# Performance work log

Measured on AMD Instinct MI355X. Metric: run time of the kernel, lower is better.

## Reference

```python
import jax, jax.numpy as jnp
from jax import lax
import numpy as np

D_IN = 512    # inputdim
HID = 128     # hiddendim
D_INNER = 2 * HID   # 256
D_PROJ = 2 * D_INNER  # 512
N_STATE = 16
R_DT = 8      # ceil(128/16)
B, H, W = 8, 32, 32


def _layernorm(y, g, b):
    mu = y.mean(-1, keepdims=True)
    var = ((y - mu) ** 2).mean(-1, keepdims=True)
    return (y - mu) / jnp.sqrt(var + 1e-5) * g + b


def _ssm(x, xw, dtw, dtb, Al, Dv, g, be):
    # x: [B, D, L] -> y: [B, L, D]  (Mamba selective scan, delta_softplus=True)
    Bb, D, L = x.shape
    n = Al.shape[1]
    xd = jnp.einsum('bdl,kd->blk', x, xw)             # [B,L,R+2N]
    dts = xd[..., :R_DT]
    Bs = xd[..., R_DT:R_DT + n]                        # [B,L,N]
    Cs = xd[..., R_DT + n:]                            # [B,L,N]
    delta = jax.nn.softplus(jnp.einsum('blr,dr->bld', dts, dtw) + dtb)  # [B,L,D]
    A = -jnp.exp(Al)                                   # [D,N]
    xt = x.transpose(0, 2, 1)                          # [B,L,D]
    dA = jnp.exp(delta[..., None] * A)                 # [B,L,D,N]
    dBx = delta[..., None] * Bs[:, :, None, :] * xt[..., None]  # [B,L,D,N]

    def step(h, inp):
        da, dbx, c = inp
        h = h * da + dbx
        return h, jnp.einsum('bdn,bn->bd', h, c)

    h0 = jnp.zeros((Bb, D, n), x.dtype)
    _, ys = lax.scan(step, h0, (dA.transpose(1, 0, 2, 3),
                                dBx.transpose(1, 0, 2, 3),
                                Cs.transpose(1, 0, 2)))
    y = ys.transpose(1, 0, 2) + xt * Dv                # [B,L,D]
    return _layernorm(y, g, be)


def _up2(y, h, w):
    Bb, L, C = y.shape
    img = y.transpose(0, 2, 1).reshape(Bb, C, h, w)
    img = jnp.repeat(jnp.repeat(img, 2, axis=2), 2, axis=3)
    return img.reshape(Bb, C, 4 * L).transpose(0, 2, 1)


def _conv1x1(x, w, b):
    return jnp.einsum('bchw,oc->bohw', x, w) + b[None, :, None, None]


def _conv2s2(x, w, b):
    out = lax.conv_general_dilated(x, w, (2, 2), 'VALID',
                                   dimension_numbers=('NCHW', 'OIHW', 'NCHW'))
    return out + b[None, :, None, None]


def _forward(input_f, in_w, in_b, c1_w, c1_b, c2_w, c2_b, c3_w, c3_b, out_w, out_b,
             xw1, dtw1, dtb1, Al1, Dv1, g1, be1,
             xw2, dtw2, dtb2, Al2, Dv2, g2, be2,
             xw3, dtw3, dtb3, Al3, Dv3, g3, be3):
    xz = _conv1x1(input_f, in_w, in_b)
    x, z = jnp.split(xz, 2, axis=1)
    f1 = _conv1x1(x, c1_w, c1_b)                      # [B,256,H,W]
    f2 = _conv2s2(f1, c2_w, c2_b)                     # [B,256,H/2,W/2]
    f3 = _conv2s2(f2, c3_w, c3_b)                     # [B,256,H/4,W/4]

    Bb, C, h3, w3 = f3.shape
    fx3 = f3.reshape(Bb, C, h3 * w3)
    y3 = _ssm(fx3, xw3, dtw3, dtb3, Al3, Dv3, g3, be3) + \
         jnp.flip(_ssm(jnp.flip(fx3, -1), xw3, dtw3, dtb3, Al3, Dv3, g3, be3), 1)
    y2_ = _up2(y3, h3, w3)

    _, _, h2, w2 = f2.shape
    fx2 = f2.reshape(Bb, C, h2 * w2)
    y2 = _ssm(fx2, xw2, dtw2, dtb2, Al2, Dv2, g2, be2) + \
         jnp.flip(_ssm(jnp.flip(fx2, -1), xw2, dtw2, dtb2, Al2, Dv2, g2, be2), 1) + y2_
    y1_ = _up2(y2, h2, w2)

    _, _, h1, w1 = f1.shape
    fx1 = f1.reshape(Bb, C, h1 * w1)
    # NOTE: source uses fssm1 forward and fssm2 on the flipped sequence
    y1 = _ssm(fx1, xw1, dtw1, dtb1, Al1, Dv1, g1, be1) + \
         jnp.flip(_ssm(jnp.flip(fx1, -1), xw2, dtw2, dtb2, Al2, Dv2, g2, be2), 1) + y1_

    out1 = y1.transpose(0, 2, 1).reshape(Bb, C, h1, w1)
    out = out1 * jax.nn.silu(z)
    return _conv1x1(out, out_w, out_b)


def setup_inputs() -> dict:
    key = jax.random.key(0)
    ks = iter(jax.random.split(key, 64))
    def nrm(shape, s=0.05):
        return (jax.random.normal(next(ks), shape, dtype=jnp.float32) * s)
    inp = {
        'input_f': jax.random.normal(next(ks), (B, D_IN, H, W), dtype=jnp.float32),
        'in_w': nrm((D_PROJ, D_IN)), 'in_b': nrm((D_PROJ,)),
        'c1_w': nrm((D_INNER, D_INNER)), 'c1_b': nrm((D_INNER,)),
        'c2_w': nrm((D_INNER, D_INNER, 2, 2)), 'c2_b': nrm((D_INNER,)),
        'c3_w': nrm((D_INNER, D_INNER, 2, 2)), 'c3_b': nrm((D_INNER,)),
        'out_w': nrm((D_IN, D_INNER)), 'out_b': nrm((D_IN,)),
    }
    Al = jnp.log(jnp.tile(jnp.arange(1, N_STATE + 1, dtype=jnp.float32), (D_INNER, 1)))
    for i in (1, 2, 3):
        inp[f'xw{i}'] = nrm((R_DT + 2 * N_STATE, D_INNER))
        inp[f'dtw{i}'] = nrm((D_INNER, R_DT), s=R_DT ** -0.5)
        inp[f'dtb{i}'] = nrm((D_INNER,)) - 4.0   # inv-softplus of small dt
        inp[f'Al{i}'] = Al
        inp[f'Dv{i}'] = jnp.ones((D_INNER,), jnp.float32)
        inp[f'g{i}'] = jnp.ones((D_INNER,), jnp.float32)
        inp[f'be{i}'] = jnp.zeros((D_INNER,), jnp.float32)
    return inp


def reference(input_f, in_w, in_b, c1_w, c1_b, c2_w, c2_b, c3_w, c3_b, out_w, out_b,
              xw1, dtw1, dtb1, Al1, Dv1, g1, be1,
              xw2, dtw2, dtb2, Al2, Dv2, g2, be2,
              xw3, dtw3, dtb3, Al3, Dv3, g3, be3):
    return _forward(input_f, in_w, in_b, c1_w, c1_b, c2_w, c2_b, c3_w, c3_b, out_w, out_b,
                    xw1, dtw1, dtb1, Al1, Dv1, g1, be1,
                    xw2, dtw2, dtb2, Al2, Dv2, g2, be2,
                    xw3, dtw3, dtb3, Al3, Dv3, g3, be3)
```

## Files before the change

kernel.cpp:

```cpp
#include <hip/hip_runtime.h>
#include <cstddef>

#define DEV static __device__ __forceinline__

typedef __attribute__((ext_vector_type(8))) short short8;
typedef __attribute__((ext_vector_type(4))) float floatx4;

DEV float siluf(float v) { return v / (1.f + expf(-v)); }

DEV unsigned short f2bf(float f) {
  unsigned int u = __float_as_uint(f);
  u += 0x7fff + ((u >> 16) & 1);
  return (unsigned short)(u >> 16);
}
DEV float bf2f(unsigned short u) {
  return __uint_as_float(((unsigned int)u) << 16);
}
DEV float4 bf2f4(ushort4 v) {
  return make_float4(bf2f(v.x), bf2f(v.y), bf2f(v.z), bf2f(v.w));
}

template <int CTRL>
DEV float qadd(float v) {
  int s = __builtin_amdgcn_update_dpp(__float_as_int(v), __float_as_int(v),
                                      CTRL, 0xF, 0xF, false);
  return v + __int_as_float(s);
}

__global__ __launch_bounds__(256) void prep_k(
    const float* __restrict__ in_w, const float* __restrict__ c1_w,
    const float* __restrict__ c2_w, const float* __restrict__ c3_w,
    const float* __restrict__ out_w, const float* __restrict__ xw1,
    const float* __restrict__ xw2, const float* __restrict__ xw3,
    unsigned short* __restrict__ wsW,
    const float* __restrict__ input_f, unsigned short* __restrict__ inT,
    const float* __restrict__ in_b, const float* __restrict__ c1_b,
    unsigned short* __restrict__ w_fz, float* __restrict__ bias_fz)
{
  __shared__ float tile[32][33];
  __shared__ float c1s[1024];
  __shared__ float part[32][8];
  int bid = blockIdx.x;
  int t = threadIdx.x;
  if (bid < 3960) {
    int gid = bid * 256 + t;
    float v;
    if      (gid < 262144)  v = in_w[gid];
    else if (gid < 327680)  v = c1_w[gid - 262144];
    else if (gid < 589824)  {
      int off = gid - 327680;
      int o = off >> 10, kk = off & 1023, ij = kk >> 8, c = kk & 255;
      v = c2_w[o * 1024 + c * 4 + ij];
    }
    else if (gid < 851968)  {
      int off = gid - 589824;
      int o = off >> 10, kk = off & 1023, ij = kk >> 8, c = kk & 255;
      v = c3_w[o * 1024 + c * 4 + ij];
    }
    else if (gid < 983040)  v = out_w[gid - 851968];
    else if (gid < 993280)  v = xw1[gid - 983040];
    else if (gid < 1003520) v = xw2[gid - 993280];
    else                    v = xw3[gid - 1003520];
    wsW[gid] = f2bf(v);
  } else if (bid < 8056) {
    int idx = bid - 3960;
    int b = idx >> 9, blk = idx & 511;
    int pt = blk & 31, ct = blk >> 5;
    int p0 = pt * 32, c0 = ct * 32;
    int r = t >> 5, cc = t & 31;
#pragma unroll
    for (int i = 0; i < 4; i++) {
      int row = r + 8 * i;
      tile[row][cc] = input_f[((size_t)b * 512 + c0 + row) * 1024 + p0 + cc];
    }
    __syncthreads();
#pragma unroll
    for (int i = 0; i < 4; i++) {
      int row = r + 8 * i;
      inT[((size_t)b * 1024 + p0 + row) * 512 + c0 + cc] = f2bf(tile[cc][row]);
    }
  } else if (bid < 8184) {
    int ib = bid - 8056;
    int ot = ib >> 1;
    int ci = ((ib & 1) << 8) + t;
#pragma unroll
    for (int rr = 0; rr < 4; rr++)
      c1s[rr * 256 + t] = c1_w[(size_t)(ot * 4 + rr) * 256 + t];
    __syncthreads();
    float acc[4] = {0.f, 0.f, 0.f, 0.f};
#pragma unroll 4
    for (int m = 0; m < 256; m++) {
      float wv = in_w[(size_t)m * 512 + ci];
#pragma unroll
      for (int rr = 0; rr < 4; rr++) acc[rr] += c1s[rr * 256 + m] * wv;
    }
#pragma unroll
    for (int rr = 0; rr < 4; rr++)
      w_fz[(size_t)(ot * 4 + rr) * 512 + ci] = f2bf(acc[rr]);
  } else if (bid < 8192) {
    int jb = bid - 8184;
    int oo = t >> 3, mc = t & 7;
    int o = jb * 32 + oo;
    float s = 0.f;
#pragma unroll 8
    for (int mm = 0; mm < 32; mm++) {
      int m = mc * 32 + mm;
      s += c1_w[(size_t)o * 256 + m] * in_b[m];
    }
    part[oo][mc] = s;
    __syncthreads();
    if (mc == 0) {
      float a = c1_b[o];
#pragma unroll
      for (int k = 0; k < 8; k++) a += part[oo][k];
      bias_fz[o] = a;
    }
    if (jb == 0) bias_fz[256 + t] = in_b[256 + t];
  } else {
    int r = bid - 8192;
    const float* src = in_w + (size_t)(256 + r) * 512;
    w_fz[(size_t)(256 + r) * 512 + t]       = f2bf(src[t]);
    w_fz[(size_t)(256 + r) * 512 + 256 + t] = f2bf(src[256 + t]);
  }
}

template <int EPI>
DEV void mgemm_body(const unsigned short* __restrict__ A, long long sA,
                    const unsigned short* __restrict__ B, long long sB,
                    const float* __restrict__ bias,
                    void* __restrict__ O1, void* __restrict__ O2,
                    void* __restrict__ O3,
                    int M, int N, int K, int Mt, int Nt, int bid)
{
  __shared__ __align__(16) unsigned short Ab[2 * 128 * 40];
  __shared__ __align__(16) unsigned short Bb[2 * 128 * 40];
  int tiles = Mt * Nt;
  int bb = bid / tiles;
  int rr = bid - bb * tiles;
  int m0 = (rr / Nt) * 128;
  int n0 = (rr % Nt) * 128;
  const unsigned short* Ap = A + (size_t)bb * sA;
  const unsigned short* Bp = B + (size_t)bb * sB;

  int t = threadIdx.x;
  int lane = t & 63;
  int wm = ((t >> 7) & 1) * 64;
  int wn = ((t >> 6) & 1) * 64;
  int l15 = lane & 15, quad = lane >> 4;

  int srow = t >> 1;
  int shalf = (t & 1) * 16;
  int arow = m0 + srow; if (arow > M - 1) arow = M - 1;
  int brow = n0 + srow; if (brow > N - 1) brow = N - 1;
  const unsigned short* ap = Ap + (size_t)arow * K + shalf;
  const unsigned short* bp = Bp + (size_t)brow * K + shalf;
  unsigned short* as = &Ab[srow * 40 + shalf];
  unsigned short* bs = &Bb[srow * 40 + shalf];

  floatx4 acc[4][4] = {};

  uint4 a0 = *(const uint4*)(ap);
  uint4 a1 = *(const uint4*)(ap + 8);
  uint4 b0 = *(const uint4*)(bp);
  uint4 b1 = *(const uint4*)(bp + 8);
  *(uint4*)as = a0; *(uint4*)(as + 8) = a1;
  *(uint4*)bs = b0; *(uint4*)(bs + 8) = b1;
  __syncthreads();
  int cur = 0;
  for (int k0 = 0; k0 < K; k0 += 32) {
    bool last = (k0 + 32 >= K);
    if (!last) {
      a0 = *(const uint4*)(ap + k0 + 32);
      a1 = *(const uint4*)(ap + k0 + 40);
      b0 = *(const uint4*)(bp + k0 + 32);
      b1 = *(const uint4*)(bp + k0 + 40);
    }
    int co = cur * 5120;
    short8 af[4], bfr[4];
#pragma unroll
    for (int i = 0; i < 4; i++)
      af[i] = *(const short8*)&Ab[co + (wm + i * 16 + l15) * 40 + quad * 8];
#pragma unroll
    for (int j = 0; j < 4; j++)
      bfr[j] = *(const short8*)&Bb[co + (wn + j * 16 + l15) * 40 + quad * 8];
#pragma unroll
    for (int i = 0; i < 4; i++)
#pragma unroll
      for (int j = 0; j < 4; j++)
        acc[i][j] = __builtin_amdgcn_mfma_f32_16x16x32_bf16(af[i], bfr[j],
                                                            acc[i][j], 0, 0, 0);
    if (!last) {
      int no = 5120 - co;
      *(uint4*)(as + no) = a0; *(uint4*)(as + no + 8) = a1;
      *(uint4*)(bs + no) = b0; *(uint4*)(bs + no + 8) = b1;
      __syncthreads();
      cur ^= 1;
    }
  }

  if (EPI == 1) {
    unsigned short* F1t = (unsigned short*)O1;
    unsigned short* F1b = (unsigned short*)O2;
    unsigned short* Sz  = (unsigned short*)O3;
    float bn[4]; int nn[4];
#pragma unroll
    for (int j = 0; j < 4; j++) { nn[j] = n0 + wn + j * 16 + l15; bn[j] = bias[nn[j]]; }
#pragma unroll
    for (int i = 0; i < 4; i++) {
      int pixb = m0 + wm + i * 16 + quad * 4;
#pragma unroll
      for (int j = 0; j < 4; j++) {
        int n = nn[j];
        float vr[4];
#pragma unroll
        for (int r = 0; r < 4; r++) vr[r] = acc[i][j][r] + bn[j];
        if (n < 256) {
#pragma unroll
          for (int r = 0; r < 4; r++)
            F1t[((size_t)bb * 1024 + pixb + r) * 256 + n] = f2bf(vr[r]);
          ushort4 o4;
          o4.x = f2bf(vr[0]); o4.y = f2bf(vr[1]); o4.z = f2bf(vr[2]); o4.w = f2bf(vr[3]);
          *(ushort4*)&F1b[((size_t)bb * 256 + n) * 1024 + pixb] = o4;
        } else {
#pragma unroll
          for (int r = 0; r < 4; r++)
            Sz[((size_t)bb * 1024 + pixb + r) * 256 + (n - 256)] =
                f2bf(siluf(vr[r]));
        }
      }
    }
  } else {
#pragma unroll
    for (int i = 0; i < 4; i++) {
      int m = m0 + wm + i * 16 + quad * 4;
#pragma unroll
      for (int j = 0; j < 4; j++) {
        int n = n0 + wn + j * 16 + l15;
        if (m < M && n < N) {
          float vr[4];
#pragma unroll
          for (int r = 0; r < 4; r++)
            vr[r] = acc[i][j][r] + (bias ? bias[m + r] : 0.f);
          float* Y0 = (float*)O1;
          float* yp = &Y0[((size_t)bb * M + m) * N + n];
#pragma unroll
          for (int r = 0; r < 4; r++) yp[(size_t)r * N] = vr[r];
        }
      }
    }
  }
}

template <int EPI>
__global__ __launch_bounds__(256) void mgemm_k(
    const unsigned short* __restrict__ A, long long sA,
    const unsigned short* __restrict__ B, long long sB,
    const float* __restrict__ bias, void* __restrict__ O1, void* __restrict__ O2,
    void* __restrict__ O3,
    int M, int N, int K, int Mt, int Nt)
{
  mgemm_body<EPI>(A, sA, B, sB, bias, O1, O2, O3, M, N, K, Mt, Nt, blockIdx.x);
}

__global__ __launch_bounds__(256) void cgemm_k(
    const unsigned short* __restrict__ A,
    const unsigned short* __restrict__ B, long long sB,
    const float* __restrict__ bias,
    unsigned short* __restrict__ O1, unsigned short* __restrict__ O2,
    int M, int N, int K, int Mt, int Nt)
{
  __shared__ __align__(16) unsigned short Ab[2][64 * 72];
  __shared__ __align__(16) unsigned short Bb[2][32 * 72];
  int bid = blockIdx.x;
  int tiles = Mt * Nt;
  int bb = bid / tiles;
  int rr = bid - bb * tiles;
  int m0 = (rr / Nt) * 64;
  int n0 = (rr % Nt) * 32;
  const unsigned short* Bp = B + (size_t)bb * sB;

  int t = threadIdx.x, lane = t & 63;
  int wm = ((t >> 7) & 1) * 32;
  int wn = ((t >> 6) & 1) * 16;
  int l15 = lane & 15, quad = lane >> 4;

  int ar = t >> 2, ac = (t & 3) * 16;
  int brc = (t >> 2) & 31, bc = (t & 3) * 16;
  const unsigned short* apc = A + (size_t)(m0 + ar) * K + ac;
  const unsigned short* bpc = Bp + (size_t)(n0 + brc) * K + bc;

  floatx4 acc2[2] = {};

  uint4 av0 = *(const uint4*)(apc);
  uint4 av1 = *(const uint4*)(apc + 8);
  uint4 bv0 = {}, bv1 = {};
  if (t < 128) { bv0 = *(const uint4*)(bpc); bv1 = *(const uint4*)(bpc + 8); }
  {
    unsigned short* asc = &Ab[0][0] + ar * 72 + ac;
    *(uint4*)asc = av0; *(uint4*)(asc + 8) = av1;
    if (t < 128) {
      unsigned short* bsc = &Bb[0][0] + brc * 72 + bc;
      *(uint4*)bsc = bv0; *(uint4*)(bsc + 8) = bv1;
    }
  }
  __syncthreads();
  int cur = 0;
  for (int k0 = 0; k0 < K; k0 += 64) {
    bool last = (k0 + 64 >= K);
    if (!last) {
      av0 = *(const uint4*)(apc + k0 + 64);
      av1 = *(const uint4*)(apc + k0 + 72);
      if (t < 128) {
        bv0 = *(const uint4*)(bpc + k0 + 64);
        bv1 = *(const uint4*)(bpc + k0 + 72);
      }
    }
    const unsigned short* Ac = &Ab[cur][0];
    const unsigned short* Bc = &Bb[cur][0];
    short8 afc[2][2], bfc[2];
#pragma unroll
    for (int i = 0; i < 2; i++)
#pragma unroll
      for (int kk = 0; kk < 2; kk++)
        afc[i][kk] = *(const short8*)&Ac[(wm + i * 16 + l15) * 72 + kk * 32 + quad * 8];
#pragma unroll
    for (int kk = 0; kk < 2; kk++)
      bfc[kk] = *(const short8*)&Bc[(wn + l15) * 72 + kk * 32 + quad * 8];
#pragma unroll
    for (int kk = 0; kk < 2; kk++) {
      acc2[0] = __builtin_amdgcn_mfma_f32_16x16x32_bf16(afc[0][kk], bfc[kk], acc2[0], 0, 0, 0);
      acc2[1] = __builtin_amdgcn_mfma_f32_16x16x32_bf16(afc[1][kk], bfc[kk], acc2[1], 0, 0, 0);
    }
    if (!last) {
      unsigned short* asn = &Ab[cur ^ 1][0] + ar * 72 + ac;
      *(uint4*)asn = av0; *(uint4*)(asn + 8) = av1;
      if (t < 128) {
        unsigned short* bsn = &Bb[cur ^ 1][0] + brc * 72 + bc;
        *(uint4*)bsn = bv0; *(uint4*)(bsn + 8) = bv1;
      }
      __syncthreads();
      cur ^= 1;
    }
  }

#pragma unroll
  for (int i = 0; i < 2; i++) {
    int m = m0 + wm + i * 16 + quad * 4;
    int n = n0 + wn + l15;
    float vr[4];
#pragma unroll
    for (int r = 0; r < 4; r++) vr[r] = acc2[i][r] + bias[m + r];
#pragma unroll
    for (int r = 0; r < 4; r++)
      O1[((size_t)bb * M + m + r) * N + n] = f2bf(vr[r]);
    ushort4 o;
    o.x = f2bf(vr[0]); o.y = f2bf(vr[1]); o.z = f2bf(vr[2]); o.w = f2bf(vr[3]);
    *(ushort4*)&O2[((size_t)bb * N + n) * M + m] = o;
  }
}

__global__ __launch_bounds__(256) void fat1_k(
    const unsigned short* __restrict__ w_xw12, const unsigned short* __restrict__ f1t,
    float* __restrict__ xd12, unsigned short* __restrict__ ic2)
{
  int bid = blockIdx.x;
  if (bid < 64) {
    mgemm_body<0>(w_xw12, 0, f1t, 1024 * 256, nullptr, xd12, nullptr, nullptr,
                  80, 1024, 256, 1, 8, bid);
  } else {
    int idx = (bid - 64) * 256 + threadIdx.x;
    int cs = idx & 31, ij = (idx >> 5) & 3, n = (idx >> 7) & 255, b = idx >> 15;
    int i = ij >> 1, j = ij & 1;
    int y = n >> 4, x = n & 15;
    int pix = (2 * y + i) * 32 + 2 * x + j;
    uint4 v = *(const uint4*)&f1t[((size_t)b * 1024 + pix) * 256 + cs * 8];
    *(uint4*)&ic2[((size_t)b * 256 + n) * 1024 + ij * 256 + cs * 8] = v;
  }
}

__global__ __launch_bounds__(256) void fat2_k(
    const unsigned short* __restrict__ w_xw2, const unsigned short* __restrict__ f2t,
    float* __restrict__ xd2, unsigned short* __restrict__ ic3)
{
  int bid = blockIdx.x;
  if (bid < 16) {
    mgemm_body<0>(w_xw2, 0, f2t, 256 * 256, nullptr, xd2, nullptr, nullptr,
                  40, 256, 256, 1, 2, bid);
  } else {
    int idx = (bid - 16) * 256 + threadIdx.x;
    int cs = idx & 31, ij = (idx >> 5) & 3, n = (idx >> 7) & 63, b = idx >> 13;
    int i = ij >> 1, j = ij & 1;
    int y = n >> 3, x = n & 7;
    int pix = (2 * y + i) * 16 + 2 * x + j;
    uint4 v = *(const uint4*)&f2t[((size_t)b * 256 + pix) * 256 + cs * 8];
    *(uint4*)&ic3[((size_t)b * 64 + n) * 1024 + ij * 256 + cs * 8] = v;
  }
}

__global__ __launch_bounds__(256) void post_all_k(
    const float* __restrict__ xd12, const float* __restrict__ xd2,
    const float* __restrict__ xd3,
    const float* __restrict__ dtw1, const float* __restrict__ dtb1,
    const float* __restrict__ dtw2, const float* __restrict__ dtb2,
    const float* __restrict__ dtw3, const float* __restrict__ dtb3,
    float* __restrict__ d1f, float* __restrict__ bc1f,
    float* __restrict__ d1b, float* __restrict__ bc1b,
    float* __restrict__ d2g, float* __restrict__ bc2,
    float* __restrict__ d3g, float* __restrict__ bc3)
{
  int bid = blockIdx.x;
  const float* xd; int bstride, L; const float *dtw, *dtb; float *dg, *bg;
  int lt, b;
  if (bid < 512) {
    int r = bid; lt = r & 63; b = r >> 6;
    xd = xd12; bstride = 80 * 1024; L = 1024; dtw = dtw1; dtb = dtb1; dg = d1f; bg = bc1f;
  } else if (bid < 1024) {
    int r = bid - 512; lt = r & 63; b = r >> 6;
    xd = xd12 + 40 * 1024; bstride = 80 * 1024; L = 1024; dtw = dtw2; dtb = dtb2; dg = d1b; bg = bc1b;
  } else if (bid < 1152) {
    int r = bid - 1024; lt = r & 15; b = r >> 4;
    xd = xd2; bstride = 40 * 256; L = 256; dtw = dtw2; dtb = dtb2; dg = d2g; bg = bc2;
  } else {
    int r = bid - 1152; lt = r & 3; b = r >> 2;
    xd = xd3; bstride = 40 * 64; L = 64; dtw = dtw3; dtb = dtb3; dg = d3g; bg = bc3;
  }
  int l0 = lt * 16;
  __shared__ float dl[8][16];
  int t = threadIdx.x;
  const float* xb = xd + (size_t)b * bstride + l0;
  if (t < 128) {
    int r = t >> 4, l = t & 15;
    dl[r][l] = xb[(size_t)r * L + l];
  } else {
    int tt = t - 128;
    int c = tt >> 2, seg = tt & 3;
    float4 v = *(const float4*)&xb[(size_t)(8 + c) * L + seg * 4];
    *(float4*)&bg[((size_t)b * 32 + c) * L + l0 + seg * 4] = v;
  }
  __syncthreads();
  int d = t;
  float dtwv[8];
#pragma unroll
  for (int r = 0; r < 8; r++) dtwv[r] = dtw[d * 8 + r];
  float dtbv = dtb[d];
  float spv[16];
#pragma unroll
  for (int l = 0; l < 16; l++) {
    float s = dtbv;
#pragma unroll
    for (int r = 0; r < 8; r++) s += dl[r][l] * dtwv[r];
    spv[l] = fmaxf(s, 0.f) + log1pf(expf(-fabsf(s)));
  }
  float* dout = dg + ((size_t)b * 256 + d) * L + l0;
#pragma unroll
  for (int i = 0; i < 4; i++)
    *(float4*)&dout[4 * i] = make_float4(spv[4 * i], spv[4 * i + 1],
                                         spv[4 * i + 2], spv[4 * i + 3]);
}

#define SCAN_STEPA(DVV, DXV, BVV) {                     \
    float e_ = __builtin_amdgcn_exp2f((DVV) * A2);      \
    h = h * e_ + (BVV) * (DXV);                         \
    S += (DVV); }

__global__ __launch_bounds__(256) void scanA_k(
    const unsigned short* __restrict__ f1b, const unsigned short* __restrict__ f2b,
    const float* __restrict__ d1f, const float* __restrict__ bc1f,
    const float* __restrict__ d1b, const float* __restrict__ bc1b,
    const float* __restrict__ d2,  const float* __restrict__ bc2,
    const float* __restrict__ Al1, const float* __restrict__ Al2,
    float* __restrict__ cP, float* __restrict__ cQ)
{
  __shared__ __align__(16) float lds[48][68];
  int bid = blockIdx.x;
  int sid, tseg, L; const unsigned short* xin; const float *dlp, *bcp, *Alp;
  if (bid < 4096) {
    sid = bid >> 4; tseg = bid & 15; L = 1024; xin = f1b;
    if (((sid >> 4) & 1) == 0) { dlp = d1f; bcp = bc1f; Alp = Al1; }
    else                       { dlp = d1b; bcp = bc1b; Alp = Al2; }
  } else {
    int idx = bid - 4096; sid = idx >> 2; tseg = idx & 3; L = 256;
    xin = f2b; dlp = d2; bcp = bc2; Alp = Al2;
  }
  int b = sid >> 5, dir = (sid >> 4) & 1, g = sid & 15;
  int t = threadIdx.x, n = t & 15, dloc = t >> 4, d = g * 16 + dloc;
  int mbase = dir ? (L - 64 * (tseg + 1)) : 64 * tseg;

  int r0 = t >> 4, cs = t & 15;
  {
    const float* p0 = dlp + ((size_t)b * 256 + g * 16 + r0) * L + mbase;
    const unsigned short* p1 = xin + ((size_t)b * 256 + g * 16 + r0) * L + mbase;
    const float* p2 = bcp + ((size_t)b * 32 + r0) * L + mbase;
    float4 v0 = *(const float4*)(p0 + cs * 4);
    float4 xf = bf2f4(*(const ushort4*)(p1 + cs * 4));
    float4 v2 = *(const float4*)(p2 + cs * 4);
    float4 dx = make_float4(v0.x * xf.x, v0.y * xf.y, v0.z * xf.z, v0.w * xf.w);
    *(float4*)&lds[r0][cs * 4]      = v0;
    *(float4*)&lds[16 + r0][cs * 4] = dx;
    *(float4*)&lds[32 + r0][cs * 4] = v2;
  }
  __syncthreads();

  float A2 = -expf(Alp[d * 16 + n]) * 1.442695040888963f;
  float h = 0.f, S = 0.f;
  if (dir == 0) {
#pragma unroll
    for (int g4 = 0; g4 < 16; g4++) {
      int cb = 4 * g4;
      float4 dv4 = *(const float4*)&lds[dloc][cb];
      float4 dx4 = *(const float4*)&lds[16 + dloc][cb];
      float4 bv4 = *(const float4*)&lds[32 + n][cb];
      SCAN_STEPA(dv4.x, dx4.x, bv4.x);
      SCAN_STEPA(dv4.y, dx4.y, bv4.y);
      SCAN_STEPA(dv4.z, dx4.z, bv4.z);
      SCAN_STEPA(dv4.w, dx4.w, bv4.w);
    }
  } else {
#pragma unroll
    for (int g4 = 0; g4 < 16; g4++) {
      int cb = 60 - 4 * g4;
      float4 dv4 = *(const float4*)&lds[dloc][cb];
      float4 dx4 = *(const float4*)&lds[16 + dloc][cb];
      float4 bv4 = *(const float4*)&lds[32 + n][cb];
      SCAN_STEPA(dv4.w, dx4.w, bv4.w);
      SCAN_STEPA(dv4.z, dx4.z, bv4.z);
      SCAN_STEPA(dv4.y, dx4.y, bv4.y);
      SCAN_STEPA(dv4.x, dx4.x, bv4.x);
    }
  }
  cP[(size_t)bid * 256 + t] = __builtin_amdgcn_exp2f(S * A2);
  cQ[(size_t)bid * 256 + t] = h;
}

__global__ __launch_bounds__(256) void scanB_k(
    const float* __restrict__ cP, const float* __restrict__ cQ,
    float* __restrict__ cH)
{
  int bid = blockIdx.x, t = threadIdx.x;
  if (bid < 256) {
    size_t base = (size_t)bid * 16 * 256 + t;
    float h = 0.f;
#pragma unroll
    for (int s = 0; s < 16; ++s) {
      size_t off = base + (size_t)s * 256;
      cH[off] = h;
      h = cP[off] * h + cQ[off];
    }
  } else {
    size_t base = (size_t)(4096 + (bid - 256) * 4) * 256 + t;
    float h = 0.f;
#pragma unroll
    for (int s = 0; s < 4; ++s) {
      size_t off = base + (size_t)s * 256;
      cH[off] = h;
      h = cP[off] * h + cQ[off];
    }
  }
}

#define QSTEP(DS, XU, CI, II) {                                         \
    float4 bv = *(const float4*)&ld_b[CI][n0];                          \
    float4 cv = *(const float4*)&ld_c[CI][n0];                          \
    float xs_ = bf2f(XU) * (DS);                                        \
    float4 e_;                                                          \
    e_.x = __builtin_amdgcn_exp2f((DS) * A4.x);                         \
    e_.y = __builtin_amdgcn_exp2f((DS) * A4.y);                         \
    e_.z = __builtin_amdgcn_exp2f((DS) * A4.z);                         \
    e_.w = __builtin_amdgcn_exp2f((DS) * A4.w);                         \
    h4.x = h4.x * e_.x + bv.x * xs_;                                    \
    h4.y = h4.y * e_.y + bv.y * xs_;                                    \
    h4.z = h4.z * e_.z + bv.z * xs_;                                    \
    h4.w = h4.w * e_.w + bv.w * xs_;                                    \
    float pp_ = h4.x * cv.x + h4.y * cv.y + h4.z * cv.z + h4.w * cv.w;  \
    pp_ = qadd<0xB1>(pp_);                                              \
    pp_ = qadd<0x4E>(pp_);                                              \
    ysel = (nq == (II)) ? pp_ : ysel; }

__global__ __launch_bounds__(256) void scanC_k(
    const unsigned short* __restrict__ f1b, const unsigned short* __restrict__ f2b,
    const unsigned short* __restrict__ f3b,
    const float* __restrict__ d1f, const float* __restrict__ bc1f,
    const float* __restrict__ d1b, const float* __restrict__ bc1b,
    const float* __restrict__ d2,  const float* __restrict__ bc2,
    const float* __restrict__ d3,  const float* __restrict__ bc3,
    float* __restrict__ y1f, float* __restrict__ y1b,
    float* __restrict__ y2f, float* __restrict__ y2b,
    float* __restrict__ y3f, float* __restrict__ y3b,
    const float* __restrict__ Al1, const float* __restrict__ Dv1,
    const float* __restrict__ Al2, const float* __restrict__ Dv2,
    const float* __restrict__ Al3, const float* __restrict__ Dv3,
    const float* __restrict__ cH)
{
  __shared__ __align__(16) unsigned short ld_xs[64][72];
  __shared__ __align__(16) float ld_b[64][20];
  __shared__ __align__(16) float ld_c[64][20];

  int bid = blockIdx.x;
  int b, dir, g4, tseg, L, lvl;
  const unsigned short* xin; const float *dlp, *bcp, *Alp, *Dvp; float* yo;
  if (bid < 1024) {
    b = bid >> 7; dir = (bid >> 6) & 1; g4 = (bid >> 4) & 3; tseg = bid & 15;
    L = 1024; xin = f1b; lvl = 1;
    if (dir == 0) { dlp = d1f; bcp = bc1f; Alp = Al1; Dvp = Dv1; yo = y1f; }
    else          { dlp = d1b; bcp = bc1b; Alp = Al2; Dvp = Dv2; yo = y1b; }
  } else if (bid < 1280) {
    int idx = bid - 1024;
    b = idx >> 5; dir = (idx >> 4) & 1; g4 = (idx >> 2) & 3; tseg = idx & 3;
    L = 256; xin = f2b; lvl = 2;
    dlp = d2; bcp = bc2; Alp = Al2; Dvp = Dv2; yo = dir ? y2b : y2f;
  } else {
    int idx = bid - 1280;
    b = idx >> 3; dir = (idx >> 2) & 1; g4 = idx & 3; tseg = 0;
    L = 64; xin = f3b; lvl = 3;
    dlp = d3; bcp = bc3; Alp = Al3; Dvp = Dv3; yo = dir ? y3b : y3f;
  }
  int mbase = dir ? (L - 64 * (tseg + 1)) : 64 * tseg;
  int t = threadIdx.x;
  int dl = t >> 2, nq = t & 3, n0 = nq * 4;
  int d = g4 * 64 + dl;

  float4 h4 = make_float4(0.f, 0.f, 0.f, 0.f);
  if (lvl != 3) {
    int gold = g4 * 4 + (dl >> 4);
    int soff = (lvl == 1) ? (b * 32 + dir * 16 + gold) * 16
                          : 4096 + (b * 32 + dir * 16 + gold) * 4;
    h4 = *(const float4*)&cH[(size_t)(soff + tseg) * 256 +
                             (size_t)((dl & 15) * 16 + n0)];
  }

  {
    int rr = t >> 2, q = t & 3;
    const unsigned short* xr = xin + ((size_t)b * 256 + g4 * 64 + rr) * L + mbase;
#pragma unroll
    for (int j = 0; j < 4; ++j) {
      int c = q * 4 + 16 * j;
      *(ushort4*)&ld_xs[rr][c] = *(const ushort4*)(xr + c);
    }
    int nn = t >> 4, c4 = t & 15;
    const float* br = bcp + ((size_t)b * 32 + nn) * L + mbase + c4 * 4;
    const float* cr = br + (size_t)16 * L;
    float4 bv = *(const float4*)br;
    float4 cv = *(const float4*)cr;
    ld_b[c4 * 4 + 0][nn] = bv.x; ld_b[c4 * 4 + 1][nn] = bv.y;
    ld_b[c4 * 4 + 2][nn] = bv.z; ld_b[c4 * 4 + 3][nn] = bv.w;
    ld_c[c4 * 4 + 0][nn] = cv.x; ld_c[c4 * 4 + 1][nn] = cv.y;
    ld_c[c4 * 4 + 2][nn] = cv.z; ld_c[c4 * 4 + 3][nn] = cv.w;
  }

  const float* drow = dlp + ((size_t)b * 256 + d) * L + mbase;

  float4 A4;
  A4.x = -expf(Alp[d * 16 + n0 + 0]) * 1.442695040888963f;
  A4.y = -expf(Alp[d * 16 + n0 + 1]) * 1.442695040888963f;
  A4.z = -expf(Alp[d * 16 + n0 + 2]) * 1.442695040888963f;
  A4.w = -expf(Alp[d * 16 + n0 + 3]) * 1.442695040888963f;
  float Dvv = Dvp[d];
  __syncthreads();

  float* ybase = yo + ((size_t)b * L + mbase) * 256 + d;
  if (dir == 0) {
#pragma unroll 1
    for (int p = 0; p < 4; ++p) {
      float yk[4];
#pragma unroll
      for (int j = 0; j < 4; ++j) {
        int cb = 16 * p + 4 * j;
        float4 dv4 = *(const float4*)(drow + cb);
        ushort4 xu4 = *(const ushort4*)&ld_xs[dl][cb];
        float ysel = 0.f;
        QSTEP(dv4.x, xu4.x, cb + 0, 0);
        QSTEP(dv4.y, xu4.y, cb + 1, 1);
        QSTEP(dv4.z, xu4.z, cb + 2, 2);
        QSTEP(dv4.w, xu4.w, cb + 3, 3);
        yk[j] = ysel;
      }
#pragma unroll
      for (int j = 0; j < 4; ++j) {
        int cst = 16 * p + 4 * j + nq;
        float xv = bf2f(ld_xs[dl][cst]);
        ybase[(size_t)cst * 256] = yk[j] + xv * Dvv;
      }
    }
  } else {
#pragma unroll 1
    for (int p = 0; p < 4; ++p) {
      float yk[4];
#pragma unroll
      for (int j = 0; j < 4; ++j) {
        int cb = 60 - 16 * p - 4 * j;
        float4 dv4 = *(const float4*)(drow + cb);
        ushort4 xu4 = *(const ushort4*)&ld_xs[dl][cb];
        float ysel = 0.f;
        QSTEP(dv4.w, xu4.w, cb + 3, 0);
        QSTEP(dv4.z, xu4.z, cb + 2, 1);
        QSTEP(dv4.y, xu4.y, cb + 1, 2);
        QSTEP(dv4.x, xu4.x, cb + 0, 3);
        yk[j] = ysel;
      }
#pragma unroll
      for (int j = 0; j < 4; ++j) {
        int cst = 60 - 16 * p - 4 * j + (3 - nq);
        float xv = bf2f(ld_xs[dl][cst]);
        ybase[(size_t)cst * 256] = yk[j] + xv * Dvv;
      }
    }
  }
}

template <int OUTBF>
__global__ __launch_bounds__(256) void ln_combine(
    const float* __restrict__ yf, const float* __restrict__ yb,
    const float* __restrict__ gf, const float* __restrict__ bef,
    const float* __restrict__ gb, const float* __restrict__ beb,
    const float* __restrict__ up, int Wc,
    const unsigned short* __restrict__ szb, void* __restrict__ outv,
    int L, int Lsh, int Wfsh)
{
  int t = threadIdx.x;
  int row = blockIdx.x * 4 + (t >> 6);
  int lane = t & 63;
  int b = row >> Lsh, l = row & (L - 1);
  size_t base = (size_t)row * 256 + lane * 4;
  float4 vf = *(const float4*)&yf[base];
  float4 vb = *(const float4*)&yb[base];
  float4 s;
  s.x = vf.x + vf.y + vf.z + vf.w;
  s.y = vf.x * vf.x + vf.y * vf.y + vf.z * vf.z + vf.w * vf.w;
  s.z = vb.x + vb.y + vb.z + vb.w;
  s.w = vb.x * vb.x + vb.y * vb.y + vb.z * vb.z + vb.w * vb.w;
#pragma unroll
  for (int m = 1; m < 64; m <<= 1) {
    s.x += __shfl_xor(s.x, m);
    s.y += __shfl_xor(s.y, m);
    s.z += __shfl_xor(s.z, m);
    s.w += __shfl_xor(s.w, m);
  }
  const float inv = 1.f / 256.f;
  float muf = s.x * inv, varf = s.y * inv - muf * muf;
  float mub = s.z * inv, varb = s.w * inv - mub * mub;
  float rf = rsqrtf(varf + 1e-5f);
  float rb = rsqrtf(varb + 1e-5f);
  int dc = lane * 4;
  float4 gfv = *(const float4*)&gf[dc];
  float4 befv = *(const float4*)&bef[dc];
  float4 gbv = *(const float4*)&gb[dc];
  float4 bebv = *(const float4*)&beb[dc];
  float4 v;
  v.x = (vf.x - muf) * rf * gfv.x + befv.x + (vb.x - mub) * rb * gbv.x + bebv.x;
  v.y = (vf.y - muf) * rf * gfv.y + befv.y + (vb.y - mub) * rb * gbv.y + bebv.y;
  v.z = (vf.z - muf) * rf * gfv.z + befv.z + (vb.z - mub) * rb * gbv.z + bebv.z;
  v.w = (vf.w - muf) * rf * gfv.w + befv.w + (vb.w - mub) * rb * gbv.w + bebv.w;
  if (up) {
    int y = l >> Wfsh, x = l & ((1 << Wfsh) - 1);
    int lc = (y >> 1) * Wc + (x >> 1);
    float4 uv = *(const float4*)&up[((size_t)b * (L >> 2) + lc) * 256 + dc];
    v.x += uv.x; v.y += uv.y; v.z += uv.z; v.w += uv.w;
  }
  if (szb) {
    ushort4 su = *(const ushort4*)&szb[base];
    v.x *= bf2f(su.x); v.y *= bf2f(su.y); v.z *= bf2f(su.z); v.w *= bf2f(su.w);
  }
  if (OUTBF) {
    ushort4 o;
    o.x = f2bf(v.x); o.y = f2bf(v.y); o.z = f2bf(v.z); o.w = f2bf(v.w);
    *(ushort4*)&((unsigned short*)outv)[base] = o;
  } else {
    *(float4*)&((float*)outv)[base] = v;
  }
}

extern "C" void kernel_launch(void* const* d_in, const int* in_sizes, int n_in,
                              void* d_out, int out_size, void* d_ws, size_t ws_size,
                              hipStream_t stream) {
  (void)in_sizes; (void)n_in; (void)out_size; (void)ws_size;
  const float* input_f = (const float*)d_in[0];
  const float* in_w  = (const float*)d_in[1];
  const float* in_b  = (const float*)d_in[2];
  const float* c1_w  = (const float*)d_in[3];
  const float* c1_b  = (const float*)d_in[4];
  const float* c2_w  = (const float*)d_in[5];
  const float* c2_b  = (const float*)d_in[6];
  const float* c3_w  = (const float*)d_in[7];
  const float* c3_b  = (const float*)d_in[8];
  const float* out_w = (const float*)d_in[9];
  const float* out_b = (const float*)d_in[10];
  const float* xw1  = (const float*)d_in[11];
  const float* dtw1 = (const float*)d_in[12];
  const float* dtb1 = (const float*)d_in[13];
  const float* Al1  = (const float*)d_in[14];
  const float* Dv1  = (const float*)d_in[15];
  const float* g1   = (const float*)d_in[16];
  const float* be1  = (const float*)d_in[17];
  const float* xw2  = (const float*)d_in[18];
  const float* dtw2 = (const float*)d_in[19];
  const float* dtb2 = (const float*)d_in[20];
  const float* Al2  = (const float*)d_in[21];
  const float* Dv2  = (const float*)d_in[22];
  const float* g2   = (const float*)d_in[23];
  const float* be2  = (const float*)d_in[24];
  const float* xw3  = (const float*)d_in[25];
  const float* dtw3 = (const float*)d_in[26];
  const float* dtb3 = (const float*)d_in[27];
  const float* Al3  = (const float*)d_in[28];
  const float* Dv3  = (const float*)d_in[29];
  const float* g3   = (const float*)d_in[30];
  const float* be3  = (const float*)d_in[31];

  float* ws = (float*)d_ws;
  constexpr size_t M1 = 2097152;
  float* d1f = ws;
  unsigned short* f1t = (unsigned short*)(ws + M1);
  float* y1f = ws + M1;
  unsigned short* szb = (unsigned short*)(ws + 2 * M1);
  unsigned short* f1b = (unsigned short*)(ws + 3 * M1);
  unsigned short* G = (unsigned short*)(ws + 3 * M1) + 2097152;
  float* d1b = ws + 4 * M1;
  unsigned short* inT = (unsigned short*)(ws + 5 * M1);
  unsigned short* ic2 = inT;
  unsigned short* ic3 = inT + 2097152;
  float* y1b = ws + 5 * M1;
  size_t o = 6 * M1;
  unsigned short* f2b = (unsigned short*)(ws + o); o += 524288;
  unsigned short* f3b = (unsigned short*)(ws + o); o += 131072;
  float* bc1f = ws + o; o += 262144;
  float* bc1b = ws + o; o += 262144;
  float* d2   = ws + o; o += 524288;
  float* bc2  = ws + o; o += 65536;
  float* d3   = ws + o; o += 131072;
  float* bc3  = ws + o; o += 16384;
  float* y2f  = ws + o; o += 524288;
  float* y2b  = ws + o; o += 524288;
  float* y3f  = ws + o; o += 131072;
  float* y3b  = ws + o; o += 131072;
  float* y3c  = ws + o; o += 131072;
  float* y2c  = ws + o; o += 524288;
  float* cP   = ws + o; o += 1310720;
  float* cQ   = ws + o; o += 1310720;
  float* cH   = ws + o; o += 1310720;
  unsigned short* wsW = (unsigned short*)(ws + o); o += 506880;
  float* bias_fz = ws + o; o += 512;
  unsigned short* w_fz = (unsigned short*)(ws + o); o += 131072;
  float* xd12 = cP;
  float* xd2  = cP + 655360;
  float* xd3  = cP + 737280;
  unsigned short* f2t = (unsigned short*)cQ;
  unsigned short* f3t = (unsigned short*)(cQ + 262144);
  unsigned short* w_c2   = wsW + 327680;
  unsigned short* w_c3   = wsW + 589824;
  unsigned short* w_out  = wsW + 851968;
  unsigned short* w_xw12 = wsW + 983040;
  unsigned short* w_xw2  = wsW + 993280;
  unsigned short* w_xw3  = wsW + 1003520;

  dim3 blk(256);

  prep_k<<<dim3(8448), blk, 0, stream>>>(in_w, c1_w, c2_w, c3_w, out_w,
                                         xw1, xw2, xw3, wsW, input_f, inT,
                                         in_b, c1_b, w_fz, bias_fz);
  mgemm_k<1><<<dim3(256), blk, 0, stream>>>(inT, 1024 * 512, w_fz, 0, bias_fz,
                                            f1t, f1b, szb, 1024, 512, 512, 8, 4);
  fat1_k<<<dim3(1088), blk, 0, stream>>>(w_xw12, f1t, xd12, ic2);
  cgemm_k<<<dim3(256), blk, 0, stream>>>(w_c2, ic2, 256 * 1024, c2_b,
                                         f2b, f2t, 256, 256, 1024, 4, 8);
  fat2_k<<<dim3(272), blk, 0, stream>>>(w_xw2, f2t, xd2, ic3);
  cgemm_k<<<dim3(64), blk, 0, stream>>>(w_c3, ic3, 64 * 1024, c3_b,
                                        f3b, f3t, 256, 64, 1024, 4, 2);
  mgemm_k<0><<<dim3(8), blk, 0, stream>>>(w_xw3, 0, f3t, 64 * 256, nullptr,
                                          xd3, nullptr, nullptr, 40, 64, 256, 1, 1);
  post_all_k<<<dim3(1184), blk, 0, stream>>>(xd12, xd2, xd3,
                                             dtw1, dtb1, dtw2, dtb2, dtw3, dtb3,
                                             d1f, bc1f, d1b, bc1b, d2, bc2, d3, bc3);
  scanA_k<<<dim3(5120), blk, 0, stream>>>(f1b, f2b, d1f, bc1f, d1b, bc1b,
                                          d2, bc2, Al1, Al2, cP, cQ);
  scanB_k<<<dim3(512), blk, 0, stream>>>(cP, cQ, cH);
  scanC_k<<<dim3(1344), blk, 0, stream>>>(f1b, f2b, f3b,
                                          d1f, bc1f, d1b, bc1b, d2, bc2, d3, bc3,
                                          y1f, y1b, y2f, y2b, y3f, y3b,
                                          Al1, Dv1, Al2, Dv2, Al3, Dv3, cH);
  ln_combine<0><<<dim3(128), blk, 0, stream>>>(y3f, y3b, g3, be3, g3, be3,
                                               nullptr, 0, nullptr, y3c, 64, 6, 3);
  ln_combine<0><<<dim3(512), blk, 0, stream>>>(y2f, y2b, g2, be2, g2, be2,
                                               y3c, 8, nullptr, y2c, 256, 8, 4);
  ln_combine<1><<<dim3(2048), blk, 0, stream>>>(y1f, y1b, g1, be1, g2, be2,
                                                y2c, 16, szb, G, 1024, 10, 5);
  mgemm_k<0><<<dim3(256), blk, 0, stream>>>(w_out, 0, G, 1024 * 256, out_b,
                                            (float*)d_out, nullptr, nullptr,
                                            512, 1024, 256, 4, 8);
}
```

Before: 316.1 us.

## Fuse delta projection and softplus into scan kernels, drop post_all_k

```diff
diff --git a/kernel.cpp b/kernel.cpp
--- a/kernel.cpp
+++ b/kernel.cpp
@@ -25,6 +25,10 @@
   int s = __builtin_amdgcn_update_dpp(__float_as_int(v), __float_as_int(v),
                                       CTRL, 0xF, 0xF, false);
   return v + __int_as_float(s);
+}
+
+DEV float softplusf(float s) {
+  return fmaxf(s, 0.f) + log1pf(expf(-fabsf(s)));
 }
 
 __global__ __launch_bounds__(256) void prep_k(
@@ -397,107 +401,64 @@
   }
 }
 
-__global__ __launch_bounds__(256) void post_all_k(
+#define SCAN_STEPA(DVV, XU, BVV) {                      \
+    float e_ = __builtin_amdgcn_exp2f((DVV) * A2);      \
+    h = h * e_ + (BVV) * ((DVV) * bf2f(XU));            \
+    S += (DVV); }
+
+__global__ __launch_bounds__(256) void scanA_k(
+    const unsigned short* __restrict__ f1b, const unsigned short* __restrict__ f2b,
     const float* __restrict__ xd12, const float* __restrict__ xd2,
-    const float* __restrict__ xd3,
     const float* __restrict__ dtw1, const float* __restrict__ dtb1,
     const float* __restrict__ dtw2, const float* __restrict__ dtb2,
-    const float* __restrict__ dtw3, const float* __restrict__ dtb3,
-    float* __restrict__ d1f, float* __restrict__ bc1f,
-    float* __restrict__ d1b, float* __restrict__ bc1b,
-    float* __restrict__ d2g, float* __restrict__ bc2,
-    float* __restrict__ d3g, float* __restrict__ bc3)
-{
-  int bid = blockIdx.x;
-  const float* xd; int bstride, L; const float *dtw, *dtb; float *dg, *bg;
-  int lt, b;
-  if (bid < 512) {
-    int r = bid; lt = r & 63; b = r >> 6;
-    xd = xd12; bstride = 80 * 1024; L = 1024; dtw = dtw1; dtb = dtb1; dg = d1f; bg = bc1f;
-  } else if (bid < 1024) {
-    int r = bid - 512; lt = r & 63; b = r >> 6;
-    xd = xd12 + 40 * 1024; bstride = 80 * 1024; L = 1024; dtw = dtw2; dtb = dtb2; dg = d1b; bg = bc1b;
-  } else if (bid < 1152) {
-    int r = bid - 1024; lt = r & 15; b = r >> 4;
-    xd = xd2; bstride = 40 * 256; L = 256; dtw = dtw2; dtb = dtb2; dg = d2g; bg = bc2;
-  } else {
-    int r = bid - 1152; lt = r & 3; b = r >> 2;
-    xd = xd3; bstride = 40 * 64; L = 64; dtw = dtw3; dtb = dtb3; dg = d3g; bg = bc3;
-  }
-  int l0 = lt * 16;
-  __shared__ float dl[8][16];
-  int t = threadIdx.x;
-  const float* xb = xd + (size_t)b * bstride + l0;
-  if (t < 128) {
-    int r = t >> 4, l = t & 15;
-    dl[r][l] = xb[(size_t)r * L + l];
-  } else {
-    int tt = t - 128;
-    int c = tt >> 2, seg = tt & 3;
-    float4 v = *(const float4*)&xb[(size_t)(8 + c) * L + seg * 4];
-    *(float4*)&bg[((size_t)b * 32 + c) * L + l0 + seg * 4] = v;
-  }
-  __syncthreads();
-  int d = t;
-  float dtwv[8];
-#pragma unroll
-  for (int r = 0; r < 8; r++) dtwv[r] = dtw[d * 8 + r];
-  float dtbv = dtb[d];
-  float spv[16];
-#pragma unroll
-  for (int l = 0; l < 16; l++) {
-    float s = dtbv;
-#pragma unroll
-    for (int r = 0; r < 8; r++) s += dl[r][l] * dtwv[r];
-    spv[l] = fmaxf(s, 0.f) + log1pf(expf(-fabsf(s)));
-  }
-  float* dout = dg + ((size_t)b * 256 + d) * L + l0;
-#pragma unroll
-  for (int i = 0; i < 4; i++)
-    *(float4*)&dout[4 * i] = make_float4(spv[4 * i], spv[4 * i + 1],
-                                         spv[4 * i + 2], spv[4 * i + 3]);
-}
-
-#define SCAN_STEPA(DVV, DXV, BVV) {                     \
-    float e_ = __builtin_amdgcn_exp2f((DVV) * A2);      \
-    h = h * e_ + (BVV) * (DXV);                         \
-    S += (DVV); }
-
-__global__ __launch_bounds__(256) void scanA_k(
-    const unsigned short* __restrict__ f1b, const unsigned short* __restrict__ f2b,
-    const float* __restrict__ d1f, const float* __restrict__ bc1f,
-    const float* __restrict__ d1b, const float* __restrict__ bc1b,
-    const float* __restrict__ d2,  const float* __restrict__ bc2,
     const float* __restrict__ Al1, const float* __restrict__ Al2,
     float* __restrict__ cP, float* __restrict__ cQ)
 {
-  __shared__ __align__(16) float lds[48][68];
+  __shared__ __align__(16) float ld_dl[16][68];
+  __shared__ __align__(16) float ld_ts[8][68];
+  __shared__ __align__(16) float ld_b[16][68];
+  __shared__ __align__(16) unsigned short ld_x[16][72];
   int bid = blockIdx.x;
-  int sid, tseg, L; const unsigned short* xin; const float *dlp, *bcp, *Alp;
+  int sid, tseg, L; const unsigned short* xin;
+  if (bid < 4096) { sid = bid >> 4; tseg = bid & 15; L = 1024; xin = f1b; }
+  else { int idx = bid - 4096; sid = idx >> 2; tseg = idx & 3; L = 256; xin = f2b; }
+  int b = sid >> 5, dir = (sid >> 4) & 1, g = sid & 15;
+  const float *xdp, *dtw, *dtbp, *Alp;
   if (bid < 4096) {
-    sid = bid >> 4; tseg = bid & 15; L = 1024; xin = f1b;
-    if (((sid >> 4) & 1) == 0) { dlp = d1f; bcp = bc1f; Alp = Al1; }
-    else                       { dlp = d1b; bcp = bc1b; Alp = Al2; }
-  } else {
-    int idx = bid - 4096; sid = idx >> 2; tseg = idx & 3; L = 256;
-    xin = f2b; dlp = d2; bcp = bc2; Alp = Al2;
-  }
-  int b = sid >> 5, dir = (sid >> 4) & 1, g = sid & 15;
+    xdp = xd12 + ((size_t)b * 80 + dir * 40) * 1024;
+    if (dir == 0) { dtw = dtw1; dtbp = dtb1; Alp = Al1; }
+    else          { dtw = dtw2; dtbp = dtb2; Alp = Al2; }
+  } else {
+    xdp = xd2 + (size_t)b * 40 * 256;
+    dtw = dtw2; dtbp = dtb2; Alp = Al2;
+  }
   int t = threadIdx.x, n = t & 15, dloc = t >> 4, d = g * 16 + dloc;
   int mbase = dir ? (L - 64 * (tseg + 1)) : 64 * tseg;
 
-  int r0 = t >> 4, cs = t & 15;
   {
-    const float* p0 = dlp + ((size_t)b * 256 + g * 16 + r0) * L + mbase;
-    const unsigned short* p1 = xin + ((size_t)b * 256 + g * 16 + r0) * L + mbase;
-    const float* p2 = bcp + ((size_t)b * 32 + r0) * L + mbase;
-    float4 v0 = *(const float4*)(p0 + cs * 4);
-    float4 xf = bf2f4(*(const ushort4*)(p1 + cs * 4));
-    float4 v2 = *(const float4*)(p2 + cs * 4);
-    float4 dx = make_float4(v0.x * xf.x, v0.y * xf.y, v0.z * xf.z, v0.w * xf.w);
-    *(float4*)&lds[r0][cs * 4]      = v0;
-    *(float4*)&lds[16 + r0][cs * 4] = dx;
-    *(float4*)&lds[32 + r0][cs * 4] = v2;
+    int r = t >> 4, cs = t & 15;
+    *(float4*)&ld_b[r][cs * 4] =
+        *(const float4*)(xdp + (size_t)(8 + r) * L + mbase + cs * 4);
+    if (t < 128)
+      *(float4*)&ld_ts[r][cs * 4] =
+          *(const float4*)(xdp + (size_t)r * L + mbase + cs * 4);
+    const unsigned short* xr = xin + ((size_t)b * 256 + g * 16 + r) * L + mbase;
+    *(ushort4*)&ld_x[r][cs * 4] = *(const ushort4*)(xr + cs * 4);
+  }
+  __syncthreads();
+  {
+    float w[8];
+#pragma unroll
+    for (int r = 0; r < 8; r++) w[r] = dtw[(size_t)d * 8 + r];
+    float bb = dtbp[d];
+#pragma unroll
+    for (int k = 0; k < 4; k++) {
+      int l = n * 4 + k;
+      float s = bb;
+#pragma unroll
+      for (int r = 0; r < 8; r++) s += ld_ts[r][l] * w[r];
+      ld_dl[dloc][l] = softplusf(s);
+    }
   }
   __syncthreads();
 
@@ -507,25 +468,25 @@
 #pragma unroll
     for (int g4 = 0; g4 < 16; g4++) {
       int cb = 4 * g4;
-      float4 dv4 = *(const float4*)&lds[dloc][cb];
-      float4 dx4 = *(const float4*)&lds[16 + dloc][cb];
-      float4 bv4 = *(const float4*)&lds[32 + n][cb];
-      SCAN_STEPA(dv4.x, dx4.x, bv4.x);
-      SCAN_STEPA(dv4.y, dx4.y, bv4.y);
-      SCAN_STEPA(dv4.z, dx4.z, bv4.z);
-      SCAN_STEPA(dv4.w, dx4.w, bv4.w);
+      float4 dv4 = *(const float4*)&ld_dl[dloc][cb];
+      ushort4 xu4 = *(const ushort4*)&ld_x[dloc][cb];
+      float4 bv4 = *(const float4*)&ld_b[n][cb];
+      SCAN_STEPA(dv4.x, xu4.x, bv4.x);
+      SCAN_STEPA(dv4.y, xu4.y, bv4.y);
+      SCAN_STEPA(dv4.z, xu4.z, bv4.z);
+      SCAN_STEPA(dv4.w, xu4.w, bv4.w);
     }
   } else {
 #pragma unroll
     for (int g4 = 0; g4 < 16; g4++) {
       int cb = 60 - 4 * g4;
-      float4 dv4 = *(const float4*)&lds[dloc][cb];
-      float4 dx4 = *(const float4*)&lds[16 + dloc][cb];
-      float4 bv4 = *(const float4*)&lds[32 + n][cb];
-      SCAN_STEPA(dv4.w, dx4.w, bv4.w);
-      SCAN_STEPA(dv4.z, dx4.z, bv4.z);
-      SCAN_STEPA(dv4.y, dx4.y, bv4.y);
-      SCAN_STEPA(dv4.x, dx4.x, bv4.x);
+      float4 dv4 = *(const float4*)&ld_dl[dloc][cb];
+      ushort4 xu4 = *(const ushort4*)&ld_x[dloc][cb];
+      float4 bv4 = *(const float4*)&ld_b[n][cb];
+      SCAN_STEPA(dv4.w, xu4.w, bv4.w);
+      SCAN_STEPA(dv4.z, xu4.z, bv4.z);
+      SCAN_STEPA(dv4.y, xu4.y, bv4.y);
+      SCAN_STEPA(dv4.x, xu4.x, bv4.x);
     }
   }
   cP[(size_t)bid * 256 + t] = __builtin_amdgcn_exp2f(S * A2);
@@ -579,10 +540,11 @@
 __global__ __launch_bounds__(256) void scanC_k(
     const unsigned short* __restrict__ f1b, const unsigned short* __restrict__ f2b,
     const unsigned short* __restrict__ f3b,
-    const float* __restrict__ d1f, const float* __restrict__ bc1f,
-    const float* __restrict__ d1b, const float* __restrict__ bc1b,
-    const float* __restrict__ d2,  const float* __restrict__ bc2,
-    const float* __restrict__ d3,  const float* __restrict__ bc3,
+    const float* __restrict__ xd12, const float* __restrict__ xd2,
+    const float* __restrict__ xd3,
+    const float* __restrict__ dtw1, const float* __restrict__ dtb1,
+    const float* __restrict__ dtw2, const float* __restrict__ dtb2,
+    const float* __restrict__ dtw3, const float* __restrict__ dtb3,
     float* __restrict__ y1f, float* __restrict__ y1b,
     float* __restrict__ y2f, float* __restrict__ y2b,
     float* __restrict__ y3f, float* __restrict__ y3b,
@@ -591,28 +553,33 @@
     const float* __restrict__ Al3, const float* __restrict__ Dv3,
     const float* __restrict__ cH)
 {
+  __shared__ __align__(16) float ld_d[64][68];
+  __shared__ __align__(16) float ld_ts[8][68];
   __shared__ __align__(16) unsigned short ld_xs[64][72];
   __shared__ __align__(16) float ld_b[64][20];
   __shared__ __align__(16) float ld_c[64][20];
 
   int bid = blockIdx.x;
   int b, dir, g4, tseg, L, lvl;
-  const unsigned short* xin; const float *dlp, *bcp, *Alp, *Dvp; float* yo;
+  const unsigned short* xin; const float *xdp, *dtw, *dtbp, *Alp, *Dvp; float* yo;
   if (bid < 1024) {
     b = bid >> 7; dir = (bid >> 6) & 1; g4 = (bid >> 4) & 3; tseg = bid & 15;
     L = 1024; xin = f1b; lvl = 1;
-    if (dir == 0) { dlp = d1f; bcp = bc1f; Alp = Al1; Dvp = Dv1; yo = y1f; }
-    else          { dlp = d1b; bcp = bc1b; Alp = Al2; Dvp = Dv2; yo = y1b; }
+    xdp = xd12 + ((size_t)b * 80 + dir * 40) * 1024;
+    if (dir == 0) { dtw = dtw1; dtbp = dtb1; Alp = Al1; Dvp = Dv1; yo = y1f; }
+    else          { dtw = dtw2; dtbp = dtb2; Alp = Al2; Dvp = Dv2; yo = y1b; }
   } else if (bid < 1280) {
     int idx = bid - 1024;
     b = idx >> 5; dir = (idx >> 4) & 1; g4 = (idx >> 2) & 3; tseg = idx & 3;
     L = 256; xin = f2b; lvl = 2;
-    dlp = d2; bcp = bc2; Alp = Al2; Dvp = Dv2; yo = dir ? y2b : y2f;
+    xdp = xd2 + (size_t)b * 40 * 256;
+    dtw = dtw2; dtbp = dtb2; Alp = Al2; Dvp = Dv2; yo = dir ? y2b : y2f;
   } else {
     int idx = bid - 1280;
     b = idx >> 3; dir = (idx >> 2) & 1; g4 = idx & 3; tseg = 0;
     L = 64; xin = f3b; lvl = 3;
-    dlp = d3; bcp = bc3; Alp = Al3; Dvp = Dv3; yo = dir ? y3b : y3f;
+    xdp = xd3 + (size_t)b * 40 * 64;
+    dtw = dtw3; dtbp = dtb3; Alp = Al3; Dvp = Dv3; yo = dir ? y3b : y3f;
   }
   int mbase = dir ? (L - 64 * (tseg + 1)) : 64 * tseg;
   int t = threadIdx.x;
@@ -637,17 +604,18 @@
       *(ushort4*)&ld_xs[rr][c] = *(const ushort4*)(xr + c);
     }
     int nn = t >> 4, c4 = t & 15;
-    const float* br = bcp + ((size_t)b * 32 + nn) * L + mbase + c4 * 4;
-    const float* cr = br + (size_t)16 * L;
+    const float* br = xdp + (size_t)(8 + nn) * L + mbase + c4 * 4;
+    const float* cr = xdp + (size_t)(24 + nn) * L + mbase + c4 * 4;
     float4 bv = *(const float4*)br;
     float4 cv = *(const float4*)cr;
     ld_b[c4 * 4 + 0][nn] = bv.x; ld_b[c4 * 4 + 1][nn] = bv.y;
     ld_b[c4 * 4 + 2][nn] = bv.z; ld_b[c4 * 4 + 3][nn] = bv.w;
     ld_c[c4 * 4 + 0][nn] = cv.x; ld_c[c4 * 4 + 1][nn] = cv.y;
     ld_c[c4 * 4 + 2][nn] = cv.z; ld_c[c4 * 4 + 3][nn] = cv.w;
-  }
-
-  const float* drow = dlp + ((size_t)b * 256 + d) * L + mbase;
+    if (t < 128)
+      *(float4*)&ld_ts[t >> 4][c4 * 4] =
+          *(const float4*)(xdp + (size_t)(t >> 4) * L + mbase + c4 * 4);
+  }
 
   float4 A4;
   A4.x = -expf(Alp[d * 16 + n0 + 0]) * 1.442695040888963f;
@@ -657,6 +625,22 @@
   float Dvv = Dvp[d];
   __syncthreads();
 
+  {
+    float w[8];
+#pragma unroll
+    for (int r = 0; r < 8; r++) w[r] = dtw[(size_t)d * 8 + r];
+    float bb = dtbp[d];
+#pragma unroll
+    for (int k = 0; k < 16; k++) {
+      int l = nq * 16 + k;
+      float s = bb;
+#pragma unroll
+      for (int r = 0; r < 8; r++) s += ld_ts[r][l] * w[r];
+      ld_d[dl][l] = softplusf(s);
+    }
+  }
+  __syncthreads();
+
   float* ybase = yo + ((size_t)b * L + mbase) * 256 + d;
   if (dir == 0) {
 #pragma unroll 1
@@ -665,7 +649,7 @@
 #pragma unroll
       for (int j = 0; j < 4; ++j) {
         int cb = 16 * p + 4 * j;
-        float4 dv4 = *(const float4*)(drow + cb);
+        float4 dv4 = *(const float4*)&ld_d[dl][cb];
         ushort4 xu4 = *(const ushort4*)&ld_xs[dl][cb];
         float ysel = 0.f;
         QSTEP(dv4.x, xu4.x, cb + 0, 0);
@@ -688,7 +672,7 @@
 #pragma unroll
       for (int j = 0; j < 4; ++j) {
         int cb = 60 - 16 * p - 4 * j;
-        float4 dv4 = *(const float4*)(drow + cb);
+        float4 dv4 = *(const float4*)&ld_d[dl][cb];
         ushort4 xu4 = *(const ushort4*)&ld_xs[dl][cb];
         float ysel = 0.f;
         QSTEP(dv4.w, xu4.w, cb + 3, 0);
@@ -808,26 +792,21 @@
 
   float* ws = (float*)d_ws;
   constexpr size_t M1 = 2097152;
-  float* d1f = ws;
+  float* xd12 = ws;
+  float* xd2  = ws + 655360;
+  float* xd3  = ws + 737280;
   unsigned short* f1t = (unsigned short*)(ws + M1);
   float* y1f = ws + M1;
   unsigned short* szb = (unsigned short*)(ws + 2 * M1);
   unsigned short* f1b = (unsigned short*)(ws + 3 * M1);
   unsigned short* G = (unsigned short*)(ws + 3 * M1) + 2097152;
-  float* d1b = ws + 4 * M1;
+  float* y1b = ws + 4 * M1;
   unsigned short* inT = (unsigned short*)(ws + 5 * M1);
   unsigned short* ic2 = inT;
   unsigned short* ic3 = inT + 2097152;
-  float* y1b = ws + 5 * M1;
   size_t o = 6 * M1;
   unsigned short* f2b = (unsigned short*)(ws + o); o += 524288;
   unsigned short* f3b = (unsigned short*)(ws + o); o += 131072;
-  float* bc1f = ws + o; o += 262144;
-  float* bc1b = ws + o; o += 262144;
-  float* d2   = ws + o; o += 524288;
-  float* bc2  = ws + o; o += 65536;
-  float* d3   = ws + o; o += 131072;
-  float* bc3  = ws + o; o += 16384;
   float* y2f  = ws + o; o += 524288;
   float* y2b  = ws + o; o += 524288;
   float* y3f  = ws + o; o += 131072;
@@ -840,9 +819,6 @@
   unsigned short* wsW = (unsigned short*)(ws + o); o += 506880;
   float* bias_fz = ws + o; o += 512;
   unsigned short* w_fz = (unsigned short*)(ws + o); o += 131072;
-  float* xd12 = cP;
-  float* xd2  = cP + 655360;
-  float* xd3  = cP + 737280;
   unsigned short* f2t = (unsigned short*)cQ;
   unsigned short* f3t = (unsigned short*)(cQ + 262144);
   unsigned short* w_c2   = wsW + 327680;
@@ -867,14 +843,12 @@
                                         f3b, f3t, 256, 64, 1024, 4, 2);
   mgemm_k<0><<<dim3(8), blk, 0, stream>>>(w_xw3, 0, f3t, 64 * 256, nullptr,
                                           xd3, nullptr, nullptr, 40, 64, 256, 1, 1);
-  post_all_k<<<dim3(1184), blk, 0, stream>>>(xd12, xd2, xd3,
-                                             dtw1, dtb1, dtw2, dtb2, dtw3, dtb3,
-                                             d1f, bc1f, d1b, bc1b, d2, bc2, d3, bc3);
-  scanA_k<<<dim3(5120), blk, 0, stream>>>(f1b, f2b, d1f, bc1f, d1b, bc1b,
-                                          d2, bc2, Al1, Al2, cP, cQ);
+  scanA_k<<<dim3(5120), blk, 0, stream>>>(f1b, f2b, xd12, xd2,
+                                          dtw1, dtb1, dtw2, dtb2,
+                                          Al1, Al2, cP, cQ);
   scanB_k<<<dim3(512), blk, 0, stream>>>(cP, cQ, cH);
-  scanC_k<<<dim3(1344), blk, 0, stream>>>(f1b, f2b, f3b,
-                                          d1f, bc1f, d1b, bc1b, d2, bc2, d3, bc3,
+  scanC_k<<<dim3(1344), blk, 0, stream>>>(f1b, f2b, f3b, xd12, xd2, xd3,
+                                          dtw1, dtb1, dtw2, dtb2, dtw3, dtb3,
                                           y1f, y1b, y2f, y2b, y3f, y3b,
                                           Al1, Dv1, Al2, Dv2, Al3, Dv3, cH);
   ln_combine<0><<<dim3(128), blk, 0, stream>>>(y3f, y3b, g3, be3, g3, be3,
```

Result: slower. 334.5 us (+5.8%).
